# Kernel optimization log

Measured on AMD Instinct MI355X. Metric: run time of the kernel, lower is better.

## Reference

```python
import jax, jax.numpy as jnp
import numpy as np

N = 65536   # batch_size * timeseries
D = 512     # feature dim of h_real
K = 64      # n_clusters


def setup_inputs() -> dict:
    key = jax.random.key(0)
    k1, k2 = jax.random.split(key)
    h_real = jax.random.normal(k1, (N, D), dtype=jnp.float32)
    # F is an (approximately) orthogonal projection parameter [N, K].
    F = jax.random.normal(k2, (N, K), dtype=jnp.float32)
    return {"h_real": h_real, "F": F}


def reference(h_real, F):
    # Original: WTW = h h^T (N x N); loss = trace(WTW) - trace(F^T WTW F).
    # Algebraically identical reduced form, never materializing the N x N Gram:
    #   trace(h h^T) = sum(h * h)
    #   trace(F^T h h^T F) = ||F^T h||_F^2
    tr_wtw = jnp.sum(h_real * h_real)
    G = F.T @ h_real                      # [K, D] skinny GEMM
    tr_proj = jnp.sum(G * G)
    return tr_wtw - tr_proj
```

## Files before the change

kernel.cpp:

```cpp
#include <hip/hip_runtime.h>
#include <hip/hip_fp16.h>
#include <hip/hip_bf16.h>

#define N_TOT 65536
#define D_DIM 512
#define K_DIM 64
#define NC    32
#define GSZ   (K_DIM * D_DIM)

typedef __bf16   bf16x8 __attribute__((ext_vector_type(8)));
typedef float    f32x4  __attribute__((ext_vector_type(4)));
typedef _Float16 half8  __attribute__((ext_vector_type(8)));

union pk4 { unsigned int u[4]; bf16x8 v; };

__device__ __forceinline__ unsigned int pack2(float a, float b) {
    __hip_bfloat162 t = __float22bfloat162_rn(make_float2(a, b));
    union { __hip_bfloat162 h; unsigned int u; } r; r.h = t;
    return r.u;
}

typedef __attribute__((address_space(3))) void       lds_void;
typedef __attribute__((address_space(1))) const void gbl_void;

__device__ __forceinline__ void dma16(const float* g, float* l) {
    __builtin_amdgcn_global_load_lds((gbl_void*)g, (lds_void*)l, 16, 0, 0);
}

extern "C" __global__ void __launch_bounds__(1024)
k1_partial(const float* __restrict__ h, const float* __restrict__ F,
           float* __restrict__ trw_out, unsigned short* __restrict__ gpart,
           float* __restrict__ out, int rowsPerBlock) {
    __shared__ float hbuf[2][NC][D_DIM];
    __shared__ float fbuf[2][NC][K_DIM];
    __shared__ float red[16];

    const int tid = threadIdx.x;
    const int b   = blockIdx.x;
    if (b == 0 && tid == 0) out[0] = 0.0f;

    const int wave = tid >> 6;
    const int lane = tid & 63;
    const int m    = lane & 15;
    const int q    = lane >> 4;

    const int row0    = b * rowsPerBlock;
    const int nChunks = rowsPerBlock / NC;

    f32x4 acc[4][2];
    #pragma unroll
    for (int kt = 0; kt < 4; ++kt)
        #pragma unroll
        for (int dt = 0; dt < 2; ++dt)
            acc[kt][dt] = (f32x4){0.f, 0.f, 0.f, 0.f};

    float trw = 0.f;

    auto stage = [&](int c, int p) {
        const int r0 = row0 + c * NC;
        const float* g = h + (size_t)(r0 + 2 * wave) * D_DIM + lane * 4;
        #pragma unroll
        for (int rr = 0; rr < 2; ++rr)
            #pragma unroll
            for (int hf = 0; hf < 2; ++hf)
                dma16(g + rr * D_DIM + hf * 256, &hbuf[p][2 * wave + rr][hf * 256]);
        if (wave < 8) {
            const float* gf = F + (size_t)(r0 + 4 * wave) * K_DIM + lane * 4;
            dma16(gf, &fbuf[p][4 * wave][0]);
        }
    };

    stage(0, 0);

    for (int c = 0; c < nChunks; ++c) {
        __syncthreads();
        if (c + 1 < nChunks) stage(c + 1, (c + 1) & 1);

        const int p = c & 1;
        bf16x8 bfrag[2], afrag[4];
        #pragma unroll
        for (int dt = 0; dt < 2; ++dt) {
            float v[8];
            #pragma unroll
            for (int j = 0; j < 8; ++j) {
                v[j] = hbuf[p][q * 8 + j][wave * 32 + dt * 16 + m];
                trw += v[j] * v[j];
            }
            pk4 pp;
            #pragma unroll
            for (int jj = 0; jj < 4; ++jj) pp.u[jj] = pack2(v[2*jj], v[2*jj+1]);
            bfrag[dt] = pp.v;
        }
        #pragma unroll
        for (int kt = 0; kt < 4; ++kt) {
            float v[8];
            #pragma unroll
            for (int j = 0; j < 8; ++j)
                v[j] = fbuf[p][q * 8 + j][kt * 16 + m];
            pk4 pp;
            #pragma unroll
            for (int jj = 0; jj < 4; ++jj) pp.u[jj] = pack2(v[2*jj], v[2*jj+1]);
            afrag[kt] = pp.v;
        }

        #pragma unroll
        for (int kt = 0; kt < 4; ++kt)
            #pragma unroll
            for (int dt = 0; dt < 2; ++dt)
                acc[kt][dt] = __builtin_amdgcn_mfma_f32_16x16x32_bf16(
                    afrag[kt], bfrag[dt], acc[kt][dt], 0, 0, 0);
    }

    unsigned short* gp = gpart + (size_t)b * GSZ;
    #pragma unroll
    for (int kt = 0; kt < 4; ++kt)
        #pragma unroll
        for (int dt = 0; dt < 2; ++dt)
            #pragma unroll
            for (int r = 0; r < 4; ++r) {
                const int k = kt * 16 + q * 4 + r;
                const int d = wave * 32 + dt * 16 + m;
                __half hv = __float2half(acc[kt][dt][r]);
                gp[k * D_DIM + d] = *(unsigned short*)&hv;
            }

    #pragma unroll
    for (int off = 32; off > 0; off >>= 1) trw += __shfl_down(trw, off, 64);
    if (lane == 0) red[wave] = trw;
    __syncthreads();
    if (tid == 0) {
        float s = 0.f;
        #pragma unroll
        for (int w = 0; w < 16; ++w) s += red[w];
        trw_out[b] = s;
    }
}

extern "C" __global__ void __launch_bounds__(512)
k2_reduce(const float* __restrict__ trw, const unsigned short* __restrict__ gpart,
          float* __restrict__ out, int P) {
    __shared__ float sh[32 * 16 * 8];
    __shared__ float red2[8];

    const int tid = threadIdx.x;
    const int sub = tid >> 4;
    const int oct = tid & 15;
    const int tt  = blockIdx.x * 16 + oct;

    float g[8];
    #pragma unroll
    for (int j = 0; j < 8; ++j) g[j] = 0.f;

    const unsigned short* base = gpart + (size_t)tt * 8;
    for (int b = sub; b < P; b += 32) {
        half8 v = *(const half8*)(base + (size_t)b * GSZ);
        #pragma unroll
        for (int j = 0; j < 8; ++j) g[j] += (float)v[j];
    }
    #pragma unroll
    for (int j = 0; j < 8; ++j) sh[(sub * 16 + oct) * 8 + j] = g[j];
    __syncthreads();

    float val = 0.f;
    if (tid < 128) {
        const int o2 = tid >> 3, j = tid & 7;
        float s = 0.f;
        #pragma unroll
        for (int sb = 0; sb < 32; ++sb) s += sh[(sb * 16 + o2) * 8 + j];
        val = -s * s;
    } else if (blockIdx.x == 0 && tid - 128 < P) {
        val = trw[tid - 128];
    }

    #pragma unroll
    for (int off = 32; off > 0; off >>= 1) val += __shfl_down(val, off, 64);
    if ((tid & 63) == 0) red2[tid >> 6] = val;
    __syncthreads();
    if (tid == 0) {
        float s = 0.f;
        #pragma unroll
        for (int w = 0; w < 8; ++w) s += red2[w];
        atomicAdd(out, s);
    }
}

extern "C" void kernel_launch(void* const* d_in, const int* in_sizes, int n_in,
                              void* d_out, int out_size, void* d_ws, size_t ws_size,
                              hipStream_t stream) {
    const float* h = (const float*)d_in[0];
    const float* F = (const float*)d_in[1];
    float* out = (float*)d_out;

    int P = 256;
    while (P > 1 && (size_t)4096 + (size_t)P * (GSZ * 2) > ws_size) P >>= 1;
    const int rowsPerBlock = N_TOT / P;

    float* trw = (float*)d_ws;
    unsigned short* gpart = (unsigned short*)((char*)d_ws + 4096);

    hipLaunchKernelGGL(k1_partial, dim3(P), dim3(1024), 0, stream,
                       h, F, trw, gpart, out, rowsPerBlock);
    hipLaunchKernelGGL(k2_reduce, dim3(256), dim3(512), 0, stream,
                       trw, gpart, out, P);
}
```

Baseline: 213.5 us.

## Single-buffer LDS, halve block size, double grid for more resident blocks

Drops the double-buffered LDS staging in favour of a single buffer with a barrier before and after compute. Each block now has 512 threads, and each wave covers 64 feature columns, so every wave holds twice as many accumulator tiles. The grid grows to 512 blocks, and the reduce kernel loops over the larger count of per-block partials. The intent is to fit several blocks per CU so they hide each other's load latency, at the cost of losing in-block prefetch overlap and doubling the partial-sum traffic for the second kernel.

```diff
diff --git a/kernel.cpp b/kernel.cpp
--- a/kernel.cpp
+++ b/kernel.cpp
@@ -7,6 +7,7 @@
 #define K_DIM 64
 #define NC    32
 #define GSZ   (K_DIM * D_DIM)
+#define NBLK  512
 
 typedef __bf16   bf16x8 __attribute__((ext_vector_type(8)));
 typedef float    f32x4  __attribute__((ext_vector_type(4)));
@@ -27,13 +28,13 @@
     __builtin_amdgcn_global_load_lds((gbl_void*)g, (lds_void*)l, 16, 0, 0);
 }
 
-extern "C" __global__ void __launch_bounds__(1024)
+extern "C" __global__ void __launch_bounds__(512, 4)
 k1_partial(const float* __restrict__ h, const float* __restrict__ F,
            float* __restrict__ trw_out, unsigned short* __restrict__ gpart,
            float* __restrict__ out, int rowsPerBlock) {
-    __shared__ float hbuf[2][NC][D_DIM];
-    __shared__ float fbuf[2][NC][K_DIM];
-    __shared__ float red[16];
+    __shared__ float hbuf[NC][D_DIM];
+    __shared__ float fbuf[NC][K_DIM];
+    __shared__ float red[8];
 
     const int tid = threadIdx.x;
     const int b   = blockIdx.x;
@@ -47,43 +48,36 @@
     const int row0    = b * rowsPerBlock;
     const int nChunks = rowsPerBlock / NC;
 
-    f32x4 acc[4][2];
+    f32x4 acc[4][4];
     #pragma unroll
     for (int kt = 0; kt < 4; ++kt)
         #pragma unroll
-        for (int dt = 0; dt < 2; ++dt)
+        for (int dt = 0; dt < 4; ++dt)
             acc[kt][dt] = (f32x4){0.f, 0.f, 0.f, 0.f};
 
     float trw = 0.f;
 
-    auto stage = [&](int c, int p) {
+    for (int c = 0; c < nChunks; ++c) {
         const int r0 = row0 + c * NC;
-        const float* g = h + (size_t)(r0 + 2 * wave) * D_DIM + lane * 4;
-        #pragma unroll
-        for (int rr = 0; rr < 2; ++rr)
-            #pragma unroll
-            for (int hf = 0; hf < 2; ++hf)
-                dma16(g + rr * D_DIM + hf * 256, &hbuf[p][2 * wave + rr][hf * 256]);
-        if (wave < 8) {
+        {
+            const float* g = h + (size_t)(r0 + 4 * wave) * D_DIM + lane * 4;
+            #pragma unroll
+            for (int rr = 0; rr < 4; ++rr)
+                #pragma unroll
+                for (int hf = 0; hf < 2; ++hf)
+                    dma16(g + rr * D_DIM + hf * 256, &hbuf[4 * wave + rr][hf * 256]);
             const float* gf = F + (size_t)(r0 + 4 * wave) * K_DIM + lane * 4;
-            dma16(gf, &fbuf[p][4 * wave][0]);
+            dma16(gf, &fbuf[4 * wave][0]);
         }
-    };
-
-    stage(0, 0);
-
-    for (int c = 0; c < nChunks; ++c) {
         __syncthreads();
-        if (c + 1 < nChunks) stage(c + 1, (c + 1) & 1);
-
-        const int p = c & 1;
-        bf16x8 bfrag[2], afrag[4];
-        #pragma unroll
-        for (int dt = 0; dt < 2; ++dt) {
+
+        bf16x8 bfrag[4], afrag[4];
+        #pragma unroll
+        for (int dt = 0; dt < 4; ++dt) {
             float v[8];
             #pragma unroll
             for (int j = 0; j < 8; ++j) {
-                v[j] = hbuf[p][q * 8 + j][wave * 32 + dt * 16 + m];
+                v[j] = hbuf[q * 8 + j][wave * 64 + dt * 16 + m];
                 trw += v[j] * v[j];
             }
             pk4 pp;
@@ -96,30 +90,31 @@
             float v[8];
             #pragma unroll
             for (int j = 0; j < 8; ++j)
-                v[j] = fbuf[p][q * 8 + j][kt * 16 + m];
+                v[j] = fbuf[q * 8 + j][kt * 16 + m];
             pk4 pp;
             #pragma unroll
             for (int jj = 0; jj < 4; ++jj) pp.u[jj] = pack2(v[2*jj], v[2*jj+1]);
             afrag[kt] = pp.v;
         }
-
         #pragma unroll
         for (int kt = 0; kt < 4; ++kt)
             #pragma unroll
-            for (int dt = 0; dt < 2; ++dt)
+            for (int dt = 0; dt < 4; ++dt)
                 acc[kt][dt] = __builtin_amdgcn_mfma_f32_16x16x32_bf16(
                     afrag[kt], bfrag[dt], acc[kt][dt], 0, 0, 0);
+
+        __syncthreads();
     }
 
     unsigned short* gp = gpart + (size_t)b * GSZ;
     #pragma unroll
     for (int kt = 0; kt < 4; ++kt)
         #pragma unroll
-        for (int dt = 0; dt < 2; ++dt)
+        for (int dt = 0; dt < 4; ++dt)
             #pragma unroll
             for (int r = 0; r < 4; ++r) {
                 const int k = kt * 16 + q * 4 + r;
-                const int d = wave * 32 + dt * 16 + m;
+                const int d = wave * 64 + dt * 16 + m;
                 __half hv = __float2half(acc[kt][dt][r]);
                 gp[k * D_DIM + d] = *(unsigned short*)&hv;
             }
@@ -131,7 +126,7 @@
     if (tid == 0) {
         float s = 0.f;
         #pragma unroll
-        for (int w = 0; w < 16; ++w) s += red[w];
+        for (int w = 0; w < 8; ++w) s += red[w];
         trw_out[b] = s;
     }
 }
@@ -168,8 +163,9 @@
         #pragma unroll
         for (int sb = 0; sb < 32; ++sb) s += sh[(sb * 16 + o2) * 8 + j];
         val = -s * s;
-    } else if (blockIdx.x == 0 && tid - 128 < P) {
-        val = trw[tid - 128];
+    } else if (blockIdx.x == 0) {
+        for (int i = tid - 128; i < P; i += 384)
+            val += trw[i];
     }
 
     #pragma unroll
@@ -191,14 +187,14 @@
     const float* F = (const float*)d_in[1];
     float* out = (float*)d_out;
 
-    int P = 256;
+    int P = NBLK;
     while (P > 1 && (size_t)4096 + (size_t)P * (GSZ * 2) > ws_size) P >>= 1;
     const int rowsPerBlock = N_TOT / P;
 
     float* trw = (float*)d_ws;
     unsigned short* gpart = (unsigned short*)((char*)d_ws + 4096);
 
-    hipLaunchKernelGGL(k1_partial, dim3(P), dim3(1024), 0, stream,
+    hipLaunchKernelGGL(k1_partial, dim3(P), dim3(512), 0, stream,
                        h, F, trw, gpart, out, rowsPerBlock);
     hipLaunchKernelGGL(k2_reduce, dim3(256), dim3(512), 0, stream,
                        trw, gpart, out, P);
```

Result: no change. 216.4 us (+1.3%).
